# Kernel tuning notes

Measured on AMD Instinct MI355X. Metric: run time of the kernel, lower is better.

## Reference

```python
import jax, jax.numpy as jnp
import numpy as np

MAX_DEG = 10
MIN_DEG = 0
N_FEAT = 128
NB_FILTER = 128
BATCH = 128
DEG_COUNT = 30000                      # atoms per degree bucket (static)
N_ATOMS = (MAX_DEG + 1) * DEG_COUNT    # 330000, atoms sorted by degree (deg0 first)
NB_AFFINE = 3 * MAX_DEG + (2 - MIN_DEG)  # 32
EPS = 1e-5


def setup_inputs() -> dict:
    key = jax.random.key(0)
    ks = jax.random.split(key, 16)
    atoms = jax.random.normal(ks[0], (N_ATOMS, N_FEAT), dtype=jnp.float32)
    membership = jax.random.randint(ks[1], (N_ATOMS,), 0, BATCH)
    # deg_slice[d] = [start, count] for degree d (atoms sorted by degree)
    deg_slice = jnp.stack([jnp.arange(MAX_DEG + 1) * DEG_COUNT,
                           jnp.full((MAX_DEG + 1,), DEG_COUNT)], axis=1)
    inp = {"atoms": atoms, "deg_slice": deg_slice, "membership": membership}
    for d in range(1, MAX_DEG + 1):
        inp[f"adj{d}"] = jax.random.randint(ks[1 + d], (DEG_COUNT, d), 0, N_ATOMS)
    glorot = (2.0 / (N_FEAT + NB_FILTER)) ** 0.5
    inp["W"] = jax.random.normal(ks[12], (NB_AFFINE, N_FEAT, NB_FILTER), dtype=jnp.float32) * glorot
    inp["b"] = jnp.zeros((NB_AFFINE, NB_FILTER), dtype=jnp.float32)
    inp["gamma"] = jnp.ones((NB_FILTER,), dtype=jnp.float32)
    inp["beta"] = jnp.zeros((NB_FILTER,), dtype=jnp.float32)
    return inp


def _self_slice(atoms, deg):
    return jax.lax.dynamic_slice_in_dim(atoms, deg * DEG_COUNT, DEG_COUNT, axis=0)


def _norm(x, gamma, beta):
    m = jnp.mean(x, axis=-1, keepdims=True)
    std = jnp.sqrt(jnp.var(x, axis=-1, keepdims=True) + EPS)
    return gamma * ((x - m) / (std + EPS)) + beta


def _forward(atoms, W, b, gamma, beta, membership, adjs):
    # W consumption order matches the TF iterator: for deg=1..max_deg -> (rel, self),
    # then deg0 self at index 2*MAX_DEG, then gather affines deg1..max_deg, deg0 last.
    rel_outs = [None] * (MAX_DEG + 1)
    gather_outs = [None] * (MAX_DEG + 1)
    for d in range(1, MAX_DEG + 1):
        neigh = jnp.sum(atoms[adjs[d - 1]], axis=1)          # (COUNT, F) gather+sum
        self_a = _self_slice(atoms, d)                        # (COUNT, F)
        i_rel, i_self = 2 * (d - 1), 2 * d - 1
        rel_outs[d] = (neigh @ W[i_rel] + b[i_rel]) + (self_a @ W[i_self] + b[i_self])
        i_g = 2 * MAX_DEG + d
        gather_outs[d] = self_a @ W[i_g] + b[i_g]
    self0 = _self_slice(atoms, 0)
    rel_outs[0] = self0 @ W[2 * MAX_DEG] + b[2 * MAX_DEG]
    gather_outs[0] = self0 @ W[NB_AFFINE - 1] + b[NB_AFFINE - 1]

    activated = jnp.concatenate(rel_outs, axis=0)             # (N_ATOMS, NB_FILTER)
    gathered = jnp.concatenate(gather_outs, axis=0)           # (N_ATOMS, NB_FILTER)
    # graph_gather: per-molecule sum (dynamic_partition + reduce_sum)
    atom_gather = jax.ops.segment_sum(gathered, membership, num_segments=BATCH)

    xn = _norm(activated, gamma, beta)                        # per-row "BN" as in source
    yn = _norm(atom_gather, gamma, beta)
    # gather_node: per-molecule max of normalized atom features
    g = jax.ops.segment_max(xn, membership, num_segments=BATCH)
    return xn, yn, g


def reference(atoms, deg_slice, membership, adj1, adj2, adj3, adj4, adj5,
              adj6, adj7, adj8, adj9, adj10, W, b, gamma, beta):
    adjs = (adj1, adj2, adj3, adj4, adj5, adj6, adj7, adj8, adj9, adj10)
    return _forward(atoms, W, b, gamma, beta, membership, adjs)
```

## Files before the change

### kernel.cpp

```cpp
#include <hip/hip_runtime.h>
#include <stdint.h>

#define MAX_DEG   10
#define DEG_COUNT 30000
#define N_ATOMS   330000
#define NF        128
#define BATCH     128
#define SORT_BLOCKS 256
#define SORT_CHUNK  1290
#define NB_BUILD  1408
#define NB_CAST   41250
#define NSLICES   8

typedef __attribute__((ext_vector_type(8))) short bf16x8;
typedef __attribute__((ext_vector_type(4))) float f32x4;
typedef __attribute__((ext_vector_type(2))) float f32x2;

__device__ __forceinline__ float bf2f(unsigned short h) {
  union { unsigned u; float f; } v; v.u = ((unsigned)h) << 16; return v.f;
}
__device__ __forceinline__ unsigned short f2bf(float f) {
  union { float f; unsigned u; } v; v.f = f;
  unsigned u = v.u;
  unsigned r = (u + 0x7fffu + ((u >> 16) & 1u)) >> 16;
  return (unsigned short)r;
}

struct AdjPtrs { const int* p[10]; };

#define NEG_INF_BITS 0xFF800000

__global__ __launch_bounds__(256) void k_prep(
    const float* __restrict__ W,
    const float* __restrict__ b,
    const f32x4* __restrict__ atoms4,
    const int* __restrict__ membership,
    unsigned short* __restrict__ BcatT,
    float* __restrict__ biascat,
    ushort4* __restrict__ dst4,
    int* __restrict__ blockHistT)
{
  const int bx = blockIdx.x;
  const int tid = threadIdx.x;
  __shared__ int bins[BATCH];

  if (bx < NB_BUILD) {
    int idx = bx * 256 + tid;
    if (idx < 11 * 128) {
      int d = idx >> 7, n = idx & 127;
      float f = (d >= 1) ? (b[(2 * (d - 1)) * 128 + n] + b[(2 * d - 1) * 128 + n])
                         : b[20 * 128 + n];
      biascat[idx] = f;
    }
    if (idx < 11 * 128 * 256) {
      int d = idx >> 15;
      int rem = idx & 32767;
      int n = rem >> 8;
      int k = rem & 255;
      float v;
      if (k < 128) {
        v = (d >= 1) ? W[(2 * (d - 1)) * 16384 + k * 128 + n] : 0.f;
      } else {
        int ks = k - 128;
        int wi = (d >= 1) ? (2 * d - 1) : 20;
        v = W[wi * 16384 + ks * 128 + n];
      }
      BcatT[idx] = f2bf(v);
    }
  } else if (bx < NB_BUILD + NB_CAST) {
    size_t i = (size_t)(bx - NB_BUILD) * 256 + tid;
    f32x4 v = __builtin_nontemporal_load(atoms4 + i);
    ushort4 o;
    o.x = f2bf(v[0]); o.y = f2bf(v[1]); o.z = f2bf(v[2]); o.w = f2bf(v[3]);
    dst4[i] = o;
  } else {
    int bh = bx - NB_BUILD - NB_CAST;
    if (tid < BATCH) bins[tid] = 0;
    __syncthreads();
    int lo = bh * SORT_CHUNK, hi = min(lo + SORT_CHUNK, N_ATOMS);
    for (int i = lo + tid; i < hi; i += 256)
      atomicAdd(&bins[membership[i]], 1);
    __syncthreads();
    if (tid < BATCH) blockHistT[tid * 256 + bh] = bins[tid];
  }
}

__global__ __launch_bounds__(256) void k_scan(
    const int* __restrict__ blockHistT,
    int* __restrict__ relOffT,
    int* __restrict__ tot)
{
  const int m = blockIdx.x;
  const int tid = threadIdx.x;
  __shared__ int ws[4];
  int v = blockHistT[m * 256 + tid];
  int x = v;
#pragma unroll
  for (int o = 1; o < 64; o <<= 1) {
    int t = __shfl_up(x, o, 64);
    if ((tid & 63) >= o) x += t;
  }
  if ((tid & 63) == 63) ws[tid >> 6] = x;
  __syncthreads();
  int wb = 0;
  for (int w = 0; w < (tid >> 6); ++w) wb += ws[w];
  int incl = wb + x;
  relOffT[m * 256 + tid] = incl - v;
  if (tid == 255) tot[m] = incl;
}

__global__ __launch_bounds__(256) void k_scatter(
    const int* __restrict__ membership,
    const int* __restrict__ relOffT,
    const int* __restrict__ tot,
    int* __restrict__ perm)
{
  __shared__ int totS[BATCH], baseS[BATCH], bins[BATCH];
  const int tid = threadIdx.x;
  if (tid < BATCH) totS[tid] = tot[tid];
  __syncthreads();
  if (tid == 0) {
    int a = 0;
    for (int i = 0; i < BATCH; ++i) { baseS[i] = a; a += totS[i]; }
  }
  __syncthreads();
  if (tid < BATCH) bins[tid] = baseS[tid] + relOffT[tid * 256 + blockIdx.x];
  __syncthreads();
  int lo = blockIdx.x * SORT_CHUNK, hi = min(lo + SORT_CHUNK, N_ATOMS);
  for (int i = lo + tid; i < hi; i += 256) {
    int m = membership[i];
    int pos = atomicAdd(&bins[m], 1);
    perm[pos] = i;
  }
}

template<int D>
__device__ __forceinline__ void nsum_phase0(const unsigned* __restrict__ atomsU,
                                            const int* __restrict__ abase,
                                            unsigned* __restrict__ NS,
                                            int rowTile, int wave, int lane) {
  for (int it = 0; it < 8; ++it) {
    int iloc = wave * 16 + it * 2;
    int r0 = rowTile * 128 + iloc;
    int sw0 = lane ^ ((iloc & 7) << 2);
    int sw1 = lane ^ (((iloc + 1) & 7) << 2);
    if (r0 < DEG_COUNT - 1) {
      const int* a = abase + (size_t)r0 * D;
      int myIdx = (lane < 2 * D) ? a[lane] : 0;
      unsigned xs[2 * D];
#pragma unroll
      for (int j = 0; j < 2 * D; ++j) {
        int nbr = __shfl(myIdx, j, 64);
        xs[j] = atomsU[(size_t)nbr * 64 + lane];
      }
      float s0a = 0.f, s1a = 0.f, s0b = 0.f, s1b = 0.f;
#pragma unroll
      for (int j = 0; j < D; ++j) {
        s0a += bf2f((unsigned short)(xs[j] & 0xffff));
        s1a += bf2f((unsigned short)(xs[j] >> 16));
      }
#pragma unroll
      for (int j = D; j < 2 * D; ++j) {
        s0b += bf2f((unsigned short)(xs[j] & 0xffff));
        s1b += bf2f((unsigned short)(xs[j] >> 16));
      }
      NS[(size_t)iloc * 64 + sw0]       = (unsigned)f2bf(s0a) | ((unsigned)f2bf(s1a) << 16);
      NS[(size_t)(iloc + 1) * 64 + sw1] = (unsigned)f2bf(s0b) | ((unsigned)f2bf(s1b) << 16);
    } else {
      const int* a = abase + (size_t)(DEG_COUNT - 1) * D;
      int myIdx = (lane < D) ? a[lane] : 0;
      unsigned xs[D];
#pragma unroll
      for (int j = 0; j < D; ++j) {
        int nbr = __shfl(myIdx, j, 64);
        xs[j] = atomsU[(size_t)nbr * 64 + lane];
      }
      float s0 = 0.f, s1 = 0.f;
#pragma unroll
      for (int j = 0; j < D; ++j) {
        s0 += bf2f((unsigned short)(xs[j] & 0xffff));
        s1 += bf2f((unsigned short)(xs[j] >> 16));
      }
      unsigned p = (unsigned)f2bf(s0) | ((unsigned)f2bf(s1) << 16);
      NS[(size_t)iloc * 64 + sw0] = p;
      NS[(size_t)(iloc + 1) * 64 + sw1] = p;
    }
  }
}

__global__ __launch_bounds__(512, 4) void k_gemm(
    const unsigned short* __restrict__ atomsBf,
    AdjPtrs adj,
    const unsigned short* __restrict__ BcatT,
    const float* __restrict__ biascat,
    const float* __restrict__ gamma,
    const float* __restrict__ beta,
    float* __restrict__ out0)
{
  const int d = blockIdx.y;
  const int rowTile = blockIdx.x;
  const int tid = threadIdx.x;
  const int lane = tid & 63;
  const int wave = tid >> 6;
  const int m16 = lane & 15;
  const int g = lane >> 4;

  __shared__ unsigned short Bs[128 * 128];
  unsigned* NS = (unsigned*)Bs;

  const unsigned short* Bd = BcatT + d * 32768;
  const unsigned* atomsU = (const unsigned*)atomsBf;

  const int rowBase = rowTile * 128 + wave * 16;
  bf16x8 af[8];
  {
    int rbL = rowBase + m16; if (rbL > DEG_COUNT - 1) rbL = DEG_COUNT - 1;
    size_t gr = (size_t)d * DEG_COUNT + rbL;
#pragma unroll
    for (int ks = 4; ks < 8; ++ks)
      af[ks] = *(const bf16x8*)(atomsBf + gr * 128 + (ks - 4) * 32 + g * 8);
  }

  if (d > 0) {
    const int* abase = adj.p[d - 1];
    switch (d) {
      case 1:  nsum_phase0<1>(atomsU, abase, NS, rowTile, wave, lane); break;
      case 2:  nsum_phase0<2>(atomsU, abase, NS, rowTile, wave, lane); break;
      case 3:  nsum_phase0<3>(atomsU, abase, NS, rowTile, wave, lane); break;
      case 4:  nsum_phase0<4>(atomsU, abase, NS, rowTile, wave, lane); break;
      case 5:  nsum_phase0<5>(atomsU, abase, NS, rowTile, wave, lane); break;
      case 6:  nsum_phase0<6>(atomsU, abase, NS, rowTile, wave, lane); break;
      case 7:  nsum_phase0<7>(atomsU, abase, NS, rowTile, wave, lane); break;
      case 8:  nsum_phase0<8>(atomsU, abase, NS, rowTile, wave, lane); break;
      case 9:  nsum_phase0<9>(atomsU, abase, NS, rowTile, wave, lane); break;
      default: nsum_phase0<10>(atomsU, abase, NS, rowTile, wave, lane); break;
    }
    __syncthreads();
    const char* nsb = (const char*)NS;
    const int rowb = (wave * 16 + m16) * 256;
    const int sw = (m16 & 7) << 4;
#pragma unroll
    for (int ks = 0; ks < 4; ++ks)
      af[ks] = *(const bf16x8*)(nsb + ((rowb + ks * 64 + g * 16) ^ sw));
  } else {
    bf16x8 z = {0, 0, 0, 0, 0, 0, 0, 0};
#pragma unroll
    for (int ks = 0; ks < 4; ++ks) af[ks] = z;
  }

  f32x4 acc[8];
#pragma unroll
  for (int ct = 0; ct < 8; ++ct) acc[ct] = (f32x4){0.f, 0.f, 0.f, 0.f};

  const int ldsMask = (m16 & 7) << 4;

#pragma unroll
  for (int h = 0; h < 2; ++h) {
    __syncthreads();
#pragma unroll
    for (int it = 0; it < 4; ++it) {
      int flat = it * 512 + tid;
      int row = flat >> 4;
      int c = flat & 15;
      uint4 v = *(const uint4*)(Bd + row * 256 + h * 128 + c * 8);
      int kb = (c * 16) ^ ((row & 7) << 4);
      *(uint4*)((char*)Bs + row * 256 + kb) = v;
    }
    __syncthreads();
#pragma unroll
    for (int ct = 0; ct < 8; ++ct) {
      const char* bbase = (const char*)Bs + (ct * 16 + m16) * 256;
      bf16x8 bf[4];
#pragma unroll
      for (int ks = 0; ks < 4; ++ks)
        bf[ks] = *(const bf16x8*)(bbase + ((ks * 64 + g * 16) ^ ldsMask));
#pragma unroll
      for (int ks = 0; ks < 4; ++ks)
        acc[ct] = __builtin_amdgcn_mfma_f32_16x16x32_bf16(af[h * 4 + ks], bf[ks], acc[ct], 0, 0, 0);
    }
  }

  float bias_[8], gam[8], bet[8];
#pragma unroll
  for (int ct = 0; ct < 8; ++ct) {
    bias_[ct] = biascat[d * 128 + ct * 16 + m16];
    gam[ct] = gamma[ct * 16 + m16];
    bet[ct] = beta[ct * 16 + m16];
  }

#pragma unroll
  for (int ct = 0; ct < 8; ++ct)
#pragma unroll
    for (int r = 0; r < 4; ++r) acc[ct][r] += bias_[ct];

  float s[4], qq[4];
#pragma unroll
  for (int r = 0; r < 4; ++r) {
    s[r] = 0.f; qq[r] = 0.f;
#pragma unroll
    for (int ct = 0; ct < 8; ++ct) {
      float v = acc[ct][r];
      s[r] += v; qq[r] += v * v;
    }
  }
#pragma unroll
  for (int off = 8; off >= 1; off >>= 1) {
#pragma unroll
    for (int r = 0; r < 4; ++r) {
      s[r]  += __shfl_xor(s[r],  off, 64);
      qq[r] += __shfl_xor(qq[r], off, 64);
    }
  }

#pragma unroll
  for (int r = 0; r < 4; ++r) {
    int rb = rowBase + g * 4 + r;
    float mean = s[r] * (1.0f / 128.0f);
    float var  = qq[r] * (1.0f / 128.0f) - mean * mean;
    float inv  = 1.0f / (sqrtf(var + 1e-5f) + 1e-5f);
    if (rb < DEG_COUNT) {
      size_t grow = (size_t)d * DEG_COUNT + rb;
#pragma unroll
      for (int ct = 0; ct < 8; ++ct)
        out0[grow * 128 + ct * 16 + m16] = gam[ct] * ((acc[ct][r] - mean) * inv) + bet[ct];
    }
  }
}

__global__ __launch_bounds__(512) void k_mreduce(
    const f32x2* __restrict__ xnV,
    const unsigned* __restrict__ atomsU,
    const int* __restrict__ perm,
    const int* __restrict__ tot,
    float* __restrict__ Spart,
    int* __restrict__ cntPart,
    float2* __restrict__ pmax4)
{
  const int m = blockIdx.x >> 3;
  const int s = blockIdx.x & 7;
  const int wave = threadIdx.x >> 6, lane = threadIdx.x & 63;

  __shared__ float S[8][11][128];
  __shared__ int C[8][11];
  __shared__ float2 maxT[8][64];
  __shared__ int totS[BATCH];
  __shared__ int rangeS[2];
  for (int e = lane; e < 11 * 128; e += 64) S[wave][e >> 7][e & 127] = 0.f;
  if (lane < 11) C[wave][lane] = 0;
  if (threadIdx.x < BATCH) totS[threadIdx.x] = tot[threadIdx.x];
  __syncthreads();
  if (threadIdx.x == 0) {
    int a = 0;
    for (int i = 0; i < m; ++i) a += totS[i];
    rangeS[0] = a; rangeS[1] = totS[m];
  }
  __syncthreads();
  const int b0 = rangeS[0], cnt = rangeS[1];
  const int lo = b0 + (cnt * s) / NSLICES;
  const int hi = b0 + (cnt * (s + 1)) / NSLICES;

  const float NEG_INF = __int_as_float((int)NEG_INF_BITS);
  float mx0 = NEG_INF, mx1 = NEG_INF;

  for (int i = lo + wave * 2; i < hi; i += 16) {
    int r0 = perm[i];
    bool has1 = (i + 1 < hi);
    int r1 = has1 ? perm[i + 1] : r0;
    f32x2 x0 = __builtin_nontemporal_load(xnV + (size_t)r0 * 64 + lane);
    unsigned a0 = __builtin_nontemporal_load(atomsU + (size_t)r0 * 64 + lane);
    f32x2 x1 = __builtin_nontemporal_load(xnV + (size_t)r1 * 64 + lane);
    unsigned a1 = __builtin_nontemporal_load(atomsU + (size_t)r1 * 64 + lane);
    int d0 = r0 / DEG_COUNT;
    mx0 = fmaxf(mx0, x0[0]);
    mx1 = fmaxf(mx1, x0[1]);
    S[wave][d0][lane]      += bf2f((unsigned short)(a0 & 0xffff));
    S[wave][d0][64 + lane] += bf2f((unsigned short)(a0 >> 16));
    if (lane == 0) C[wave][d0]++;
    if (has1) {
      int d1 = r1 / DEG_COUNT;
      mx0 = fmaxf(mx0, x1[0]);
      mx1 = fmaxf(mx1, x1[1]);
      S[wave][d1][lane]      += bf2f((unsigned short)(a1 & 0xffff));
      S[wave][d1][64 + lane] += bf2f((unsigned short)(a1 >> 16));
      if (lane == 0) C[wave][d1]++;
    }
  }
  maxT[wave][lane] = make_float2(mx0, mx1);
  __syncthreads();

  if (threadIdx.x < 64) {
    int l = threadIdx.x;
    float2 mm = maxT[0][l];
#pragma unroll
    for (int w = 1; w < 8; ++w) {
      float2 b = maxT[w][l]; mm.x = fmaxf(mm.x, b.x); mm.y = fmaxf(mm.y, b.y);
    }
    pmax4[((size_t)s * 128 + m) * 64 + l] = mm;
  }
  for (int e = threadIdx.x; e < 11 * 128; e += 512) {
    int d = e >> 7, p = e & 127;
    float t = 0.f;
#pragma unroll
    for (int w = 0; w < 8; ++w) t += S[w][d][p];
    int col = (p < 64) ? (2 * p) : (2 * (p - 64) + 1);
    Spart[(((size_t)s * 128 + m) * 11 + d) * 128 + col] = t;
  }
  if (threadIdx.x < 11) {
    int t = 0;
#pragma unroll
    for (int w = 0; w < 8; ++w) t += C[w][threadIdx.x];
    cntPart[((size_t)s * 128 + m) * 11 + threadIdx.x] = t;
  }
}

__global__ __launch_bounds__(128) void k_ynfinal(
    const float* __restrict__ Spart,
    const int* __restrict__ cntPart,
    const float* __restrict__ W,
    const float* __restrict__ b,
    const float* __restrict__ gamma,
    const float* __restrict__ beta,
    const float* __restrict__ pmax4,
    float* __restrict__ out1,
    float* __restrict__ out2)
{
  int m = blockIdx.x;
  int j = threadIdx.x;

  float g = __int_as_float((int)NEG_INF_BITS);
#pragma unroll
  for (int sl = 0; sl < NSLICES; ++sl)
    g = fmaxf(g, pmax4[((size_t)sl * 128 + m) * 128 + j]);
  out2[m * 128 + j] = g;

  __shared__ float Sm[11][128];
  __shared__ float cw[11];
  for (int e = j; e < 11 * 128; e += 128) {
    int d = e >> 7, c = e & 127;
    float t = 0.f;
#pragma unroll
    for (int sl = 0; sl < NSLICES; ++sl)
      t += Spart[(((size_t)sl * 128 + m) * 11 + d) * 128 + c];
    Sm[d][c] = t;
  }
  if (j < 11) {
    int t = 0;
#pragma unroll
    for (int sl = 0; sl < NSLICES; ++sl)
      t += cntPart[((size_t)sl * 128 + m) * 11 + j];
    cw[j] = (float)t;
  }
  __syncthreads();

  float acc = 0.f;
  for (int d = 0; d < 11; ++d) {
    int wi = (d >= 1) ? (20 + d) : 31;
    const float* Wd = W + wi * 16384;
    float a0 = 0.f, a1 = 0.f, a2 = 0.f, a3 = 0.f;
    for (int k = 0; k < 128; k += 4) {
      a0 += Sm[d][k]     * Wd[k * 128 + j];
      a1 += Sm[d][k + 1] * Wd[(k + 1) * 128 + j];
      a2 += Sm[d][k + 2] * Wd[(k + 2) * 128 + j];
      a3 += Sm[d][k + 3] * Wd[(k + 3) * 128 + j];
    }
    acc += (a0 + a1) + (a2 + a3);
    acc += cw[d] * b[wi * 128 + j];
  }

  float ws_ = acc, wq = acc * acc;
#pragma unroll
  for (int off = 32; off >= 1; off >>= 1) {
    ws_ += __shfl_xor(ws_, off, 64);
    wq  += __shfl_xor(wq, off, 64);
  }
  __shared__ float red[4];
  int wave = j >> 6, lane = j & 63;
  if (lane == 0) { red[wave * 2] = ws_; red[wave * 2 + 1] = wq; }
  __syncthreads();
  float Ssum = red[0] + red[2], Q = red[1] + red[3];
  float mean = Ssum * (1.f / 128.f);
  float var = Q * (1.f / 128.f) - mean * mean;
  float inv = 1.f / (sqrtf(var + 1e-5f) + 1e-5f);
  out1[m * 128 + j] = gamma[j] * ((acc - mean) * inv) + beta[j];
}

extern "C" void kernel_launch(void* const* d_in, const int* in_sizes, int n_in,
                              void* d_out, int out_size, void* d_ws, size_t ws_size,
                              hipStream_t stream) {
  const float* atoms = (const float*)d_in[0];
  const int* membership = (const int*)d_in[2];
  AdjPtrs adj;
  for (int i = 0; i < 10; ++i) adj.p[i] = (const int*)d_in[3 + i];
  const float* W     = (const float*)d_in[13];
  const float* b     = (const float*)d_in[14];
  const float* gamma = (const float*)d_in[15];
  const float* beta  = (const float*)d_in[16];

  char* ws = (char*)d_ws;
  size_t off = 0;
  unsigned short* atomsBf = (unsigned short*)(ws + off); off += (size_t)N_ATOMS * 128 * 2;
  unsigned short* BcatT   = (unsigned short*)(ws + off); off += (size_t)11 * 128 * 256 * 2;
  float* biascat          = (float*)(ws + off);          off += (size_t)11 * 128 * 4;
  int* perm               = (int*)(ws + off);            off += (size_t)N_ATOMS * 4;
  int* tot                = (int*)(ws + off);            off += 512;
  int* blockHistT         = (int*)(ws + off);            off += (size_t)BATCH * SORT_BLOCKS * 4;
  int* relOffT            = (int*)(ws + off);            off += (size_t)BATCH * SORT_BLOCKS * 4;
  float* Spart            = (float*)(ws + off);          off += (size_t)NSLICES * 128 * 11 * 128 * 4;
  int* cntPart            = (int*)(ws + off);            off += (size_t)NSLICES * 128 * 11 * 4;
  float* pmax4            = (float*)(ws + off);          off += (size_t)NSLICES * 128 * 128 * 4;

  float* out0 = (float*)d_out;
  float* out1 = out0 + (size_t)N_ATOMS * 128;
  float* out2 = out1 + 16384;

  hipLaunchKernelGGL(k_prep, dim3(NB_BUILD + NB_CAST + SORT_BLOCKS), dim3(256), 0, stream,
                     W, b, (const f32x4*)atoms, membership,
                     BcatT, biascat, (ushort4*)atomsBf, blockHistT);
  hipLaunchKernelGGL(k_scan, dim3(128), dim3(256), 0, stream, blockHistT, relOffT, tot);
  hipLaunchKernelGGL(k_scatter, dim3(SORT_BLOCKS), dim3(256), 0, stream,
                     membership, relOffT, tot, perm);
  hipLaunchKernelGGL(k_gemm, dim3(236, 11), dim3(512), 0, stream,
                     atomsBf, adj, BcatT, biascat, gamma, beta, out0);
  hipLaunchKernelGGL(k_mreduce, dim3(128 * NSLICES), dim3(512), 0, stream,
                     (const f32x2*)out0, (const unsigned*)atomsBf, perm, tot,
                     Spart, cntPart, (float2*)pmax4);
  hipLaunchKernelGGL(k_ynfinal, dim3(128), dim3(128), 0, stream,
                     Spart, cntPart, W, b, gamma, beta, pmax4, out1, out2);
}
```

Before: 508.8 us.

## Gather four neighbor rows per wave step and stage full weight tile once

```diff
diff --git a/kernel.cpp b/kernel.cpp
--- a/kernel.cpp
+++ b/kernel.cpp
@@ -10,7 +10,7 @@
 #define SORT_CHUNK  1290
 #define NB_BUILD  1408
 #define NB_CAST   41250
-#define NSLICES   8
+#define NSLICES   4
 
 typedef __attribute__((ext_vector_type(8))) short bf16x8;
 typedef __attribute__((ext_vector_type(4))) float f32x4;
@@ -135,55 +135,64 @@
 }
 
 template<int D>
+__device__ __forceinline__ void nsum_row1(const unsigned* __restrict__ atomsU,
+                                          const int* __restrict__ abase,
+                                          unsigned* __restrict__ NS,
+                                          int iloc, int rclamp, int lane) {
+  const int* a = abase + (size_t)rclamp * D;
+  int myIdx = (lane < D) ? a[lane] : 0;
+  unsigned xs[D];
+#pragma unroll
+  for (int j = 0; j < D; ++j) {
+    int nbr = __shfl(myIdx, j, 64);
+    xs[j] = atomsU[(size_t)nbr * 64 + lane];
+  }
+  float s0 = 0.f, s1 = 0.f;
+#pragma unroll
+  for (int j = 0; j < D; ++j) {
+    s0 += bf2f((unsigned short)(xs[j] & 0xffff));
+    s1 += bf2f((unsigned short)(xs[j] >> 16));
+  }
+  int sw = lane ^ ((iloc & 7) << 2);
+  NS[(size_t)iloc * 64 + sw] = (unsigned)f2bf(s0) | ((unsigned)f2bf(s1) << 16);
+}
+
+template<int D>
 __device__ __forceinline__ void nsum_phase0(const unsigned* __restrict__ atomsU,
                                             const int* __restrict__ abase,
                                             unsigned* __restrict__ NS,
                                             int rowTile, int wave, int lane) {
-  for (int it = 0; it < 8; ++it) {
-    int iloc = wave * 16 + it * 2;
+  for (int it = 0; it < 4; ++it) {
+    int iloc = wave * 16 + it * 4;
     int r0 = rowTile * 128 + iloc;
-    int sw0 = lane ^ ((iloc & 7) << 2);
-    int sw1 = lane ^ (((iloc + 1) & 7) << 2);
-    if (r0 < DEG_COUNT - 1) {
+    if (r0 + 3 < DEG_COUNT) {
       const int* a = abase + (size_t)r0 * D;
-      int myIdx = (lane < 2 * D) ? a[lane] : 0;
-      unsigned xs[2 * D];
-#pragma unroll
-      for (int j = 0; j < 2 * D; ++j) {
+      int myIdx = (lane < 4 * D) ? a[lane] : 0;
+      unsigned xs[4 * D];
+#pragma unroll
+      for (int j = 0; j < 4 * D; ++j) {
         int nbr = __shfl(myIdx, j, 64);
         xs[j] = atomsU[(size_t)nbr * 64 + lane];
       }
-      float s0a = 0.f, s1a = 0.f, s0b = 0.f, s1b = 0.f;
-#pragma unroll
-      for (int j = 0; j < D; ++j) {
-        s0a += bf2f((unsigned short)(xs[j] & 0xffff));
-        s1a += bf2f((unsigned short)(xs[j] >> 16));
+#pragma unroll
+      for (int rr = 0; rr < 4; ++rr) {
+        float s0 = 0.f, s1 = 0.f;
+#pragma unroll
+        for (int j = rr * D; j < (rr + 1) * D; ++j) {
+          s0 += bf2f((unsigned short)(xs[j] & 0xffff));
+          s1 += bf2f((unsigned short)(xs[j] >> 16));
+        }
+        int il = iloc + rr;
+        int sw = lane ^ ((il & 7) << 2);
+        NS[(size_t)il * 64 + sw] = (unsigned)f2bf(s0) | ((unsigned)f2bf(s1) << 16);
       }
-#pragma unroll
-      for (int j = D; j < 2 * D; ++j) {
-        s0b += bf2f((unsigned short)(xs[j] & 0xffff));
-        s1b += bf2f((unsigned short)(xs[j] >> 16));
+    } else {
+#pragma unroll
+      for (int rr = 0; rr < 4; ++rr) {
+        int r = r0 + rr;
+        int rc = (r > DEG_COUNT - 1) ? (DEG_COUNT - 1) : r;
+        nsum_row1<D>(atomsU, abase, NS, iloc + rr, rc, lane);
       }
-      NS[(size_t)iloc * 64 + sw0]       = (unsigned)f2bf(s0a) | ((unsigned)f2bf(s1a) << 16);
-      NS[(size_t)(iloc + 1) * 64 + sw1] = (unsigned)f2bf(s0b) | ((unsigned)f2bf(s1b) << 16);
-    } else {
-      const int* a = abase + (size_t)(DEG_COUNT - 1) * D;
-      int myIdx = (lane < D) ? a[lane] : 0;
-      unsigned xs[D];
-#pragma unroll
-      for (int j = 0; j < D; ++j) {
-        int nbr = __shfl(myIdx, j, 64);
-        xs[j] = atomsU[(size_t)nbr * 64 + lane];
-      }
-      float s0 = 0.f, s1 = 0.f;
-#pragma unroll
-      for (int j = 0; j < D; ++j) {
-        s0 += bf2f((unsigned short)(xs[j] & 0xffff));
-        s1 += bf2f((unsigned short)(xs[j] >> 16));
-      }
-      unsigned p = (unsigned)f2bf(s0) | ((unsigned)f2bf(s1) << 16);
-      NS[(size_t)iloc * 64 + sw0] = p;
-      NS[(size_t)(iloc + 1) * 64 + sw1] = p;
     }
   }
 }
@@ -205,7 +214,7 @@
   const int m16 = lane & 15;
   const int g = lane >> 4;
 
-  __shared__ unsigned short Bs[128 * 128];
+  __shared__ unsigned short Bs[128 * 256];
   unsigned* NS = (unsigned*)Bs;
 
   const unsigned short* Bd = BcatT + d * 32768;
@@ -242,42 +251,41 @@
 #pragma unroll
     for (int ks = 0; ks < 4; ++ks)
       af[ks] = *(const bf16x8*)(nsb + ((rowb + ks * 64 + g * 16) ^ sw));
+    __syncthreads();
   } else {
     bf16x8 z = {0, 0, 0, 0, 0, 0, 0, 0};
 #pragma unroll
     for (int ks = 0; ks < 4; ++ks) af[ks] = z;
   }
 
+#pragma unroll
+  for (int it = 0; it < 8; ++it) {
+    int flat = it * 512 + tid;
+    int row = flat >> 5;
+    int c = flat & 31;
+    uint4 v = *(const uint4*)(Bd + row * 256 + c * 8);
+    int kb = (c * 16) ^ ((row & 7) << 4);
+    *(uint4*)((char*)Bs + row * 512 + kb) = v;
+  }
+
+  __syncthreads();
+
+  const int ldsMask = (m16 & 7) << 4;
+
   f32x4 acc[8];
 #pragma unroll
   for (int ct = 0; ct < 8; ++ct) acc[ct] = (f32x4){0.f, 0.f, 0.f, 0.f};
 
-  const int ldsMask = (m16 & 7) << 4;
-
-#pragma unroll
-  for (int h = 0; h < 2; ++h) {
-    __syncthreads();
-#pragma unroll
-    for (int it = 0; it < 4; ++it) {
-      int flat = it * 512 + tid;
-      int row = flat >> 4;
-      int c = flat & 15;
-      uint4 v = *(const uint4*)(Bd + row * 256 + h * 128 + c * 8);
-      int kb = (c * 16) ^ ((row & 7) << 4);
-      *(uint4*)((char*)Bs + row * 256 + kb) = v;
-    }
-    __syncthreads();
-#pragma unroll
-    for (int ct = 0; ct < 8; ++ct) {
-      const char* bbase = (const char*)Bs + (ct * 16 + m16) * 256;
-      bf16x8 bf[4];
-#pragma unroll
-      for (int ks = 0; ks < 4; ++ks)
-        bf[ks] = *(const bf16x8*)(bbase + ((ks * 64 + g * 16) ^ ldsMask));
-#pragma unroll
-      for (int ks = 0; ks < 4; ++ks)
-        acc[ct] = __builtin_amdgcn_mfma_f32_16x16x32_bf16(af[h * 4 + ks], bf[ks], acc[ct], 0, 0, 0);
-    }
+#pragma unroll
+  for (int ct = 0; ct < 8; ++ct) {
+    const char* bbase = (const char*)Bs + (ct * 16 + m16) * 512;
+    bf16x8 bf[8];
+#pragma unroll
+    for (int ks = 0; ks < 8; ++ks)
+      bf[ks] = *(const bf16x8*)(bbase + ((ks * 64 + g * 16) ^ ldsMask));
+#pragma unroll
+    for (int ks = 0; ks < 8; ++ks)
+      acc[ct] = __builtin_amdgcn_mfma_f32_16x16x32_bf16(af[ks], bf[ks], acc[ct], 0, 0, 0);
   }
 
   float bias_[8], gam[8], bet[8];
@@ -336,8 +344,8 @@
     int* __restrict__ cntPart,
     float2* __restrict__ pmax4)
 {
-  const int m = blockIdx.x >> 3;
-  const int s = blockIdx.x & 7;
+  const int m = blockIdx.x >> 2;
+  const int s = blockIdx.x & 3;
   const int wave = threadIdx.x >> 6, lane = threadIdx.x & 63;
 
   __shared__ float S[8][11][128];
```

New measurement: 492.5 us. 1.03x faster.
